# Kernel optimization log

Measured on AMD Instinct MI355X. Metric: run time of the kernel, lower is better.

The kernel has to match this reference:

```python
import jax, jax.numpy as jnp
import numpy as np

NS = [65536, 16384, 4096, 1024, 256, 64]          # nodes per level (64 = 8 graphs x 8 dense voxels)
ES = [1048576, 262144, 65536, 16384, 4096]        # edges per level (avg degree 16)
INS = [1, 15, 23, 31, 39]
OUTS = [12, 20, 28, 36, 44]
K = 5                                             # kernel_size


def setup_inputs():
    keys = iter(jax.random.split(jax.random.key(0), 64))
    d = {'x': jax.random.normal(next(keys), (NS[0], 1), jnp.float32),
         'pos': jax.random.uniform(next(keys), (NS[0], 3), jnp.float32)}
    for l in range(5):
        n, e, ci, co = NS[l], ES[l], INS[l], OUTS[l]
        d[f'src{l}'] = jax.random.randint(next(keys), (e,), 0, n)
        d[f'dst{l}'] = jax.random.randint(next(keys), (e,), 0, n)
        d[f'eattr{l}'] = jax.random.normal(next(keys), (e, 3), jnp.float32)
        d[f'cluster{l}'] = jax.random.randint(next(keys), (n,), 0, NS[l + 1])
        d[f'w1_{l}'] = jax.random.normal(next(keys), (3, K), jnp.float32) * 0.5
        d[f'b1_{l}'] = jnp.zeros((K,), jnp.float32)
        d[f'w2_{l}'] = jax.random.normal(next(keys), (K, ci * co), jnp.float32) / np.float32(np.sqrt(K * ci))
        d[f'b2_{l}'] = jnp.zeros((ci * co,), jnp.float32)
        d[f'root_{l}'] = jax.random.normal(next(keys), (ci, co), jnp.float32) / np.float32(np.sqrt(ci))
        d[f'bias_{l}'] = jnp.zeros((co,), jnp.float32)
    d['fc_w'] = jax.random.normal(next(keys), (8 * 47, 10), jnp.float32) / np.float32(np.sqrt(8 * 47))
    d['fc_b'] = jnp.zeros((10,), jnp.float32)
    return d


def _conv(x, src, dst, eattr, w1, b1, w2, b2, root, bias, n):
    # edge-conditioned kernel: MLP(edge_attr) -> [E, ci, co]
    h = jnp.tanh(eattr @ w1 + b1)                                  # [E, K]
    We = (h @ w2 + b2).reshape(eattr.shape[0], x.shape[1], -1)     # [E, ci, co]
    msg = jnp.einsum('ei,eio->eo', x[src], We)                     # gather + per-edge matvec
    s = jax.ops.segment_sum(msg, dst, num_segments=n)
    cnt = jax.ops.segment_sum(jnp.ones((dst.shape[0], 1), x.dtype), dst, num_segments=n)
    agg = s / jnp.maximum(cnt, 1.0)                                # mean aggregation
    return agg + x @ root + bias, jnp.mean(jnp.square(We))


def _pool(x, pos, cluster, n_next):
    # sparse voxel max pool on features, mean on positions; pos concatenated to features
    xm = jax.ops.segment_max(x, cluster, num_segments=n_next)
    xm = jnp.where(jnp.isfinite(xm), xm, 0.0)                      # empty voxels -> 0
    ps = jax.ops.segment_sum(pos, cluster, num_segments=n_next)
    cnt = jax.ops.segment_sum(jnp.ones((pos.shape[0], 1), pos.dtype), cluster, num_segments=n_next)
    pm = ps / jnp.maximum(cnt, 1.0)
    return jnp.concatenate([xm, pm], axis=1), pm


def reference(x, pos, src0, dst0, eattr0, cluster0, w1_0, b1_0, w2_0, b2_0, root_0, bias_0,
              src1, dst1, eattr1, cluster1, w1_1, b1_1, w2_1, b2_1, root_1, bias_1,
              src2, dst2, eattr2, cluster2, w1_2, b1_2, w2_2, b2_2, root_2, bias_2,
              src3, dst3, eattr3, cluster3, w1_3, b1_3, w2_3, b2_3, root_3, bias_3,
              src4, dst4, eattr4, cluster4, w1_4, b1_4, w2_4, b2_4, root_4, bias_4,
              fc_w, fc_b):
    lv = [(src0, dst0, eattr0, cluster0, w1_0, b1_0, w2_0, b2_0, root_0, bias_0),
          (src1, dst1, eattr1, cluster1, w1_1, b1_1, w2_1, b2_1, root_1, bias_1),
          (src2, dst2, eattr2, cluster2, w1_2, b1_2, w2_2, b2_2, root_2, bias_2),
          (src3, dst3, eattr3, cluster3, w1_3, b1_3, w2_3, b2_3, root_3, bias_3),
          (src4, dst4, eattr4, cluster4, w1_4, b1_4, w2_4, b2_4, root_4, bias_4)]
    closs = jnp.float32(0.0)
    for l, (src, dst, ea, cl, w1, b1, w2, b2, rt, bs) in enumerate(lv):
        x, c = _conv(x, src, dst, ea, w1, b1, w2, b2, rt, bs, NS[l])
        closs = closs + c
        x, pos = _pool(x, pos, cl, NS[l + 1])
    feat = x.reshape(-1, 8 * 47)                                   # [B, 8*47]
    logits = feat @ fc_w + fc_b
    return jax.nn.log_softmax(logits, axis=1), closs
```

## Files before the change

kernel.cpp:

```cpp
#include <hip/hip_runtime.h>
#include <hip/hip_fp16.h>
#include <math.h>


#define NT0   512
#define TSZ0  2048
#define NBK0  256
#define CAP0  4608
#define NT1   128
#define TSZ1  2048
#define NBK1  256
#define CAP1  1280

__device__ __forceinline__ float ftanh(float x) {
    float e = __expf(2.f * x);
    return 1.f - 2.f / (e + 1.f);
}

__device__ __forceinline__ unsigned fenc(float f) {
    int b = __float_as_int(f);
    return (b < 0) ? ~(unsigned)b : ((unsigned)b | 0x80000000u);
}
__device__ __forceinline__ float fdec(unsigned u) {
    int b = (u & 0x80000000u) ? (int)(u & 0x7fffffffu) : ~(int)u;
    return __int_as_float(b);
}

__device__ __forceinline__ float row_val(const unsigned* __restrict__ row,
                                         int i, int CI) {
    float cn = __uint_as_float(row[CI]);
    if (i < CI - 3) return (cn == 0.f) ? 0.f : fdec(row[i]);
    return __uint_as_float(row[i]) / fmaxf(cn, 1.f);
}

struct Seg4 {
    const int* idx[4];
    int*       cnt[4];
    int*       rp [4];
    int*       out[4];
    int        n  [4];
    int        nb [4];
    int        tstart[5];
};

struct GA {
    const int *src0, *dst0; const float* ea0;
    const int *src1, *dst1; const float* ea1;
    const float *x0, *pos0;
    const int* cluster[5];
    const float *w1[5], *b1[5], *w2[5], *b2[5], *root[5], *bias[5];
    const int* srcE[3]; const float* eaE[3];
    const float *fc_w, *fc_b;
    int *bcnt, *bcnt1;
    float4 *pay2, *pay1, *rec1;
    float *y0, *xn0;
    unsigned* raw[5];
    float *H, *sq;
    int *bs1, *rp1;
    Seg4 sg;
    float* out;
    int hb0[4], hsB;
};

__global__ __launch_bounds__(256) void k1_fuseA(GA A)
{
    __shared__ float4 stg[TSZ0];
    __shared__ unsigned char bkb[TSZ0];
    __shared__ int hb_[256], gb_[256], ls_[256], cu_[256];

    int B = blockIdx.x, t = threadIdx.x;

    if (B < NT0) {
        hb_[t] = 0;
        __syncthreads();
        int base = B * TSZ0 + t;
        int dreg[8];
        #pragma unroll
        for (int k = 0; k < 8; k++) {
            dreg[k] = A.dst0[base + k * 256];
            atomicAdd(&hb_[dreg[k] >> 8], 1);
        }
        __syncthreads();
        int c = hb_[t];
        gb_[t] = c ? atomicAdd(&A.bcnt[t], c) : 0;
        ls_[t] = c;
        __syncthreads();
        for (int d = 1; d < 256; d <<= 1) {
            int u = (t >= d) ? ls_[t - d] : 0;
            __syncthreads();
            ls_[t] += u;
            __syncthreads();
        }
        int ex = ls_[t] - c;
        ls_[t] = ex;
        cu_[t] = ex;
        __syncthreads();

        float w1r[15], b1r[5];
        #pragma unroll
        for (int i = 0; i < 15; i++) w1r[i] = A.w1[0][i];
        #pragma unroll
        for (int i = 0; i < 5; i++)  b1r[i] = A.b1[0][i];
        float acc[20];
        #pragma unroll
        for (int i = 0; i < 20; i++) acc[i] = 0.f;
        #pragma unroll
        for (int k = 0; k < 8; k++) {
            int i = base + k * 256;
            int d = dreg[k];
            int sv = A.src0[i];
            float e0 = A.ea0[i * 3], e1 = A.ea0[i * 3 + 1], e2 = A.ea0[i * 3 + 2];
            float h[5];
            #pragma unroll
            for (int q = 0; q < 5; q++)
                h[q] = ftanh(e0 * w1r[q] + e1 * w1r[5 + q] + e2 * w1r[10 + q] + b1r[q]);
            int p = 5;
            #pragma unroll
            for (int q = 0; q < 5; q++) {
                acc[q] += h[q];
                #pragma unroll
                for (int q2 = q; q2 < 5; q2++) acc[p++] += h[q] * h[q2];
            }
            float xv = A.x0[sv];
            union HU { __half2 h2; float f; } p01, p23;
            p01.h2 = __floats2half2_rn(h[0], h[1]);
            p23.h2 = __floats2half2_rn(h[2], h[3]);
            unsigned wbits = ((unsigned)d << 16) |
                             (unsigned)__half_as_ushort(__float2half_rn(h[4]));
            int bk = d >> 8;
            int ps = atomicAdd(&cu_[bk], 1);
            stg[ps] = make_float4(xv, p01.f, p23.f, __uint_as_float(wbits));
            bkb[ps] = (unsigned char)bk;
        }
        __syncthreads();
        #pragma unroll
        for (int k = 0; k < 8; k++) {
            int p = k * 256 + t;
            int bk = bkb[p];
            int off = gb_[bk] + (p - ls_[bk]);
            if (off < CAP0)
                A.pay2[(size_t)bk * CAP0 + off] = stg[p];
        }
        __syncthreads();
        float* red = (float*)cu_;
        int wid = t >> 6, lane = t & 63;
        #pragma unroll
        for (int v = 0; v < 20; v++) {
            float s = acc[v];
            #pragma unroll
            for (int o = 32; o; o >>= 1) s += __shfl_down(s, o);
            if (lane == 0) red[wid * 20 + v] = s;
        }
        __syncthreads();
        if (t < 20)
            atomicAdd(&A.H[t], red[t] + red[20 + t] + red[40 + t] + red[60 + t]);
        return;
    }
    B -= NT0;
    if (B < NT1) {
        hb_[t] = 0;
        __syncthreads();
        int base = B * TSZ1 + t;
        int dreg[8];
        #pragma unroll
        for (int k = 0; k < 8; k++) {
            dreg[k] = A.dst1[base + k * 256];
            atomicAdd(&hb_[dreg[k] >> 6], 1);
        }
        __syncthreads();
        int c = hb_[t];
        gb_[t] = c ? atomicAdd(&A.bcnt1[t], c) : 0;
        ls_[t] = c;
        __syncthreads();
        for (int d = 1; d < 256; d <<= 1) {
            int u = (t >= d) ? ls_[t - d] : 0;
            __syncthreads();
            ls_[t] += u;
            __syncthreads();
        }
        int ex = ls_[t] - c;
        ls_[t] = ex;
        cu_[t] = ex;
        __syncthreads();

        float w1r[15], b1r[5];
        #pragma unroll
        for (int i = 0; i < 15; i++) w1r[i] = A.w1[1][i];
        #pragma unroll
        for (int i = 0; i < 5; i++)  b1r[i] = A.b1[1][i];
        float acc[20];
        #pragma unroll
        for (int i = 0; i < 20; i++) acc[i] = 0.f;
        #pragma unroll
        for (int k = 0; k < 8; k++) {
            int i = base + k * 256;
            int d = dreg[k];
            int sv = A.src1[i];
            float e0 = A.ea1[i * 3], e1 = A.ea1[i * 3 + 1], e2 = A.ea1[i * 3 + 2];
            float h[5];
            #pragma unroll
            for (int q = 0; q < 5; q++)
                h[q] = ftanh(e0 * w1r[q] + e1 * w1r[5 + q] + e2 * w1r[10 + q] + b1r[q]);
            int p = 5;
            #pragma unroll
            for (int q = 0; q < 5; q++) {
                acc[q] += h[q];
                #pragma unroll
                for (int q2 = q; q2 < 5; q2++) acc[p++] += h[q] * h[q2];
            }
            int bk = d >> 6;
            int ps = atomicAdd(&cu_[bk], 1);
            stg[ps] = make_float4(__int_as_float((d << 16) | sv), e0, e1, e2);
            bkb[ps] = (unsigned char)bk;
        }
        __syncthreads();
        #pragma unroll
        for (int k = 0; k < 8; k++) {
            int p = k * 256 + t;
            int bk = bkb[p];
            int off = gb_[bk] + (p - ls_[bk]);
            if (off < CAP1)
                A.pay1[(size_t)bk * CAP1 + off] = stg[p];
        }
        __syncthreads();
        float* red = (float*)cu_;
        int wid = t >> 6, lane = t & 63;
        #pragma unroll
        for (int v = 0; v < 20; v++) {
            float s = acc[v];
            #pragma unroll
            for (int o = 32; o; o >>= 1) s += __shfl_down(s, o);
            if (lane == 0) red[wid * 20 + v] = s;
        }
        __syncthreads();
        if (t < 20)
            atomicAdd(&A.H[20 + t], red[t] + red[20 + t] + red[40 + t] + red[60 + t]);
        return;
    }
    B -= NT1;
    if (B < A.hsB) {
        const int K = 8;
        int j = 0;
        while (j < 2 && B >= A.hb0[j + 1]) j++;
        int bloc = B - A.hb0[j];
        const float* ea = A.eaE[j];
        const float* w1p = A.w1[j + 2];
        const float* b1p = A.b1[j + 2];
        static const int EJ[3] = {65536, 16384, 4096};
        int Ej = EJ[j];
        float w1r[15], b1r[5];
        #pragma unroll
        for (int i = 0; i < 15; i++) w1r[i] = w1p[i];
        #pragma unroll
        for (int i = 0; i < 5; i++)  b1r[i] = b1p[i];
        float acc[20];
        #pragma unroll
        for (int i = 0; i < 20; i++) acc[i] = 0.f;
        int base = bloc * 256 * K + t;
        for (int it = 0; it < K; it++) {
            int e = base + it * 256;
            if (e < Ej) {
                float e0 = ea[e * 3], e1 = ea[e * 3 + 1], e2 = ea[e * 3 + 2];
                float h[5];
                #pragma unroll
                for (int q = 0; q < 5; q++)
                    h[q] = ftanh(e0 * w1r[q] + e1 * w1r[5 + q] + e2 * w1r[10 + q] + b1r[q]);
                int p = 5;
                #pragma unroll
                for (int q = 0; q < 5; q++) {
                    acc[q] += h[q];
                    #pragma unroll
                    for (int q2 = q; q2 < 5; q2++) acc[p++] += h[q] * h[q2];
                }
            }
        }
        float* red = (float*)hb_;
        int wid = t >> 6, lane = t & 63;
        #pragma unroll
        for (int v = 0; v < 20; v++) {
            float s = acc[v];
            #pragma unroll
            for (int o = 32; o; o >>= 1) s += __shfl_down(s, o);
            if (lane == 0) red[wid * 20 + v] = s;
        }
        __syncthreads();
        if (t < 20)
            atomicAdd(&A.H[(j + 2) * 20 + t],
                      red[t] + red[20 + t] + red[40 + t] + red[60 + t]);
        return;
    }
    B -= A.hsB;
    {
        int s = 0;
        while (s < 3 && B >= A.sg.tstart[s + 1]) s++;
        int i0 = (B - A.sg.tstart[s]) * 1024;
        const int* idx = A.sg.idx[s];
        int* cnt = A.sg.cnt[s];
        int n = A.sg.n[s];
        #pragma unroll
        for (int j = 0; j < 4; j++) {
            int i = i0 + j * 256 + t;
            if (i < n) atomicAdd(&cnt[idx[i]], 1);
        }
    }
}

__global__ __launch_bounds__(256) void k2_fuseB(GA A)
{
    __shared__ float wsm[96];
    __shared__ float nacc[7 * NBK0];
    __shared__ int sc[256];
    int B = blockIdx.x, t = threadIdx.x;

    if (B < NBK0) {
        if (t < 60) wsm[t] = A.w2[0][t];
        else if (t >= 64  && t < 76)  wsm[60 + t - 64]  = A.b2[0][t - 64];
        else if (t >= 128 && t < 140) wsm[72 + t - 128] = A.root[0][t - 128];
        else if (t >= 192 && t < 204) wsm[84 + t - 192] = A.bias[0][t - 192];
        for (int u = t; u < 7 * NBK0; u += 256) nacc[u] = 0.f;
        __syncthreads();

        int n = A.bcnt[B];
        if (n > CAP0) n = CAP0;
        size_t base = (size_t)B * CAP0;
        for (int j = t; j < n; j += 256) {
            float4 R = A.pay2[base + j];
            union HU { float f; __half2 h2; } a01, a23;
            a01.f = R.y; a23.f = R.z;
            unsigned wbits = __float_as_uint(R.w);
            int rel = (int)(wbits >> 16) & 255;
            float xv = R.x;
            atomicAdd(&nacc[rel], xv);
            atomicAdd(&nacc[256 + rel],  __low2float(a01.h2)  * xv);
            atomicAdd(&nacc[512 + rel],  __high2float(a01.h2) * xv);
            atomicAdd(&nacc[768 + rel],  __low2float(a23.h2)  * xv);
            atomicAdd(&nacc[1024 + rel], __high2float(a23.h2) * xv);
            atomicAdd(&nacc[1280 + rel],
                      __half2float(__ushort_as_half((unsigned short)(wbits & 0xffffu))) * xv);
            atomicAdd(&nacc[1536 + rel], 1.f);
        }
        __syncthreads();

        int v0 = B << 8;
        for (int u = t; u < NBK0 * 12; u += 256) {
            int rel = u / 12, o = u - rel * 12;
            float dg = nacc[1536 + rel];
            float inv = 1.f / fmaxf(dg, 1.f);
            float msg = wsm[60 + o] * nacc[rel] + wsm[o] * nacc[256 + rel] +
                        wsm[12 + o] * nacc[512 + rel] + wsm[24 + o] * nacc[768 + rel] +
                        wsm[36 + o] * nacc[1024 + rel] + wsm[48 + o] * nacc[1280 + rel];
            float xv = A.x0[v0 + rel];
            A.y0[(size_t)(v0 + rel) * 12 + o] =
                msg * inv + xv * wsm[72 + o] + wsm[84 + o];
        }
        return;
    }
    B -= NBK0;
    if (B < 1) {
        int c = A.bcnt1[t];
        if (c > CAP1) c = CAP1;
        sc[t] = c;
        __syncthreads();
        for (int d = 1; d < 256; d <<= 1) {
            int u = (t >= d) ? sc[t - d] : 0;
            __syncthreads();
            sc[t] += u;
            __syncthreads();
        }
        A.bs1[t] = sc[t] - c;
        if (t == 255) { A.bs1[256] = sc[255]; A.rp1[16384] = sc[255]; }
        return;
    }
    B -= 1;
    if (B < 4) {
        int s = B;
        int nb = A.sg.nb[s];
        const int* cnt = A.sg.cnt[s];
        int* rp = A.sg.rp[s];
        int VPT = nb >> 8;
        int i0 = t * VPT;
        int sum = 0;
        for (int k = 0; k < VPT; k++) sum += cnt[i0 + k];
        int acc = sum;
        sc[t] = acc;
        __syncthreads();
        for (int d = 1; d < 256; d <<= 1) {
            int t2 = (t >= d) ? sc[t - d] : 0;
            __syncthreads();
            acc += t2;
            sc[t] = acc;
            __syncthreads();
        }
        int running = acc - sum;
        for (int k = 0; k < VPT; k++) {
            rp[i0 + k] = running;
            running += cnt[i0 + k];
        }
        if (t == 255) rp[nb] = running;
        return;
    }
    B -= 4;
    {
        if (t >= 64) return;
        int l = B;
        const float* w2l = A.w2[l];
        const float* b2l = A.b2[l];
        static const int cicoA[5] = {12, 300, 644, 1116, 1716};
        int cico = cicoA[l];
        float d[21];
        #pragma unroll
        for (int i = 0; i < 21; i++) d[i] = 0.f;
        for (int u = t; u < cico; u += 64) {
            float b = b2l[u];
            float w[5];
            #pragma unroll
            for (int k = 0; k < 5; k++) w[k] = w2l[k * cico + u];
            int p = 0;
            #pragma unroll
            for (int k = 0; k < 5; k++) {
                #pragma unroll
                for (int k2 = k; k2 < 5; k2++) d[p++] += w[k] * w[k2];
            }
            #pragma unroll
            for (int k = 0; k < 5; k++) d[15 + k] += b * w[k];
            d[20] += b * b;
        }
        #pragma unroll
        for (int i = 0; i < 21; i++) {
            #pragma unroll
            for (int off = 32; off; off >>= 1) d[i] += __shfl_down(d[i], off);
        }
        if (t == 0) {
            static const int EA[5] = {1048576, 262144, 65536, 16384, 4096};
            const float* H1 = A.H + l * 20;
            const float* H2 = H1 + 5;
            float sq = (float)EA[l] * d[20];
            #pragma unroll
            for (int k = 0; k < 5; k++) sq += 2.f * d[15 + k] * H1[k];
            int p = 0;
            #pragma unroll
            for (int k = 0; k < 5; k++) {
                #pragma unroll
                for (int k2 = k; k2 < 5; k2++) {
                    sq += ((k == k2) ? 1.f : 2.f) * d[p] * H2[p];
                    p++;
                }
            }
            A.sq[l] = sq;
        }
    }
}

__global__ __launch_bounds__(256) void k3_fuseC(GA A)
{
    __shared__ float4 st4[CAP1];
    __shared__ short  inv[CAP1];
    __shared__ int h64[64], l64[64], c64[64];
    int B = blockIdx.x, t = threadIdx.x;

    if (B < A.sg.tstart[4]) {
        int s = 0;
        while (s < 3 && B >= A.sg.tstart[s + 1]) s++;
        int i0 = (B - A.sg.tstart[s]) * 1024;
        const int* idx = A.sg.idx[s];
        int* cnt = A.sg.cnt[s];
        const int* rp = A.sg.rp[s];
        int* out = A.sg.out[s];
        int n = A.sg.n[s];
        #pragma unroll
        for (int j = 0; j < 4; j++) {
            int i = i0 + j * 256 + t;
            if (i < n) {
                int d = idx[i];
                int p = atomicSub(&cnt[d], 1) - 1;
                out[rp[d] + p] = i;
            }
        }
        return;
    }
    B -= A.sg.tstart[4];
    {
        int b = B;
        int n = A.bcnt1[b];
        if (n > CAP1) n = CAP1;
        size_t base = (size_t)b * CAP1;
        for (int j = t; j < n; j += 256) st4[j] = A.pay1[base + j];
        if (t < 64) h64[t] = 0;
        __syncthreads();
        for (int j = t; j < n; j += 256) {
            int rel = (int)(__float_as_uint(st4[j].x) >> 16) & 63;
            atomicAdd(&h64[rel], 1);
        }
        __syncthreads();
        if (t < 64) {
            int v = h64[t];
            int val = v;
            #pragma unroll
            for (int d = 1; d < 64; d <<= 1) {
                int u = __shfl_up(val, d);
                if (t >= d) val += u;
            }
            l64[t] = val - v;
            c64[t] = val - v;
        }
        __syncthreads();
        for (int j = t; j < n; j += 256) {
            int rel = (int)(__float_as_uint(st4[j].x) >> 16) & 63;
            int p = atomicAdd(&c64[rel], 1);
            inv[p] = (short)j;
        }
        __syncthreads();
        int lo = A.bs1[b];
        for (int j = t; j < n; j += 256)
            A.rec1[lo + j] = st4[inv[j]];
        if (t < 64) A.rp1[(b << 6) + t] = lo + l64[t];
    }
}

__global__ __launch_bounds__(256) void k4_pool0(GA A)
{
    int gt = blockIdx.x * 256 + threadIdx.x;
    if (gt >= 16384 * 15) return;
    int c = gt / 15, o = gt - c * 15;
    int r0 = A.sg.rp[3][c], r1 = A.sg.rp[3][c + 1];
    const int* cnid = A.sg.out[3];
    int d = r1 - r0;
    if (o < 12) {
        float m = -INFINITY;
        for (int j = r0; j < r1; j++)
            m = fmaxf(m, A.y0[(size_t)cnid[j] * 12 + o]);
        if (d == 0 || !isfinite(m)) m = 0.f;
        A.xn0[c * 15 + o] = m;
    } else {
        int k = o - 12;
        float sum = 0.f;
        for (int j = r0; j < r1; j++)
            sum += A.pos0[cnid[j] * 3 + k];
        A.xn0[c * 15 + o] = sum / fmaxf((float)d, 1.f);
    }
}

__global__ __launch_bounds__(256) void k5_conv1(GA A)
{
    constexpr int CI = 15, CO = 20, CH = 48, CICO = CI * CO, RN = 24;
    __shared__ float w1s[20];
    __shared__ float4 recb[CH];
    __shared__ int   svb[CH];
    __shared__ float hb[CH * 6];
    __shared__ float xs[CH * CI];
    __shared__ float Sx[6 * CI];
    __shared__ float xown[CI];

    int t = threadIdx.x, v = blockIdx.x;
    if (t < 20) w1s[t] = (t < 15) ? A.w1[1][t] : A.b1[1][t - 15];
    if (t < CI) xown[t] = A.xn0[v * CI + t];
    int r0 = A.rp1[v], r1 = A.rp1[v + 1];
    int d = r1 - r0;
    float acc = 0.f;

    for (int c0 = r0; c0 < r1; c0 += CH) {
        int cn = min(CH, r1 - c0);
        if (t < cn) {
            float4 R = A.rec1[c0 + t];
            recb[t] = R;
            svb[t]  = (int)(__float_as_uint(R.x) & 0xffffu);
            hb[t * 6] = 1.f;
        }
        __syncthreads();
        if (t < cn * 5) {
            int j = t / 5, k = t % 5;
            float e0 = recb[j].y, e1 = recb[j].z, e2 = recb[j].w;
            hb[j * 6 + 1 + k] =
                ftanh(e0 * w1s[k] + e1 * w1s[5 + k] + e2 * w1s[10 + k] + w1s[15 + k]);
        }
        for (int u = t; u < cn * CI; u += 256) {
            int j = u / CI, i = u - j * CI;
            xs[u] = A.xn0[svb[j] * CI + i];
        }
        __syncthreads();
        if (t < 6 * CI) {
            int i = t / 6, k6 = t - (t / 6) * 6;
            for (int j = 0; j < cn; j++)
                acc += hb[j * 6 + k6] * xs[j * CI + i];
        }
        __syncthreads();
    }

    if (t < 6 * CI) Sx[t] = acc;
    __syncthreads();

    if (t < CO) {
        float m = 0.f;
        const float* w2 = A.w2[1];
        const float* b2 = A.b2[1];
        for (int i = 0; i < CI; i++) {
            m += b2[i * CO + t] * Sx[i * 6];
            #pragma unroll
            for (int k = 0; k < 5; k++)
                m += w2[k * CICO + i * CO + t] * Sx[i * 6 + 1 + k];
        }
        m /= fmaxf((float)d, 1.f);
        for (int i = 0; i < CI; i++) m += xown[i] * A.root[1][i * CO + t];
        m += A.bias[1][t];
        int c = A.cluster[1][v];
        unsigned* orow = A.raw[1] + (size_t)c * RN;
        atomicMax(&orow[t], fenc(m));
        if (t < 3) atomicAdd((float*)&orow[CO + t], xown[CI - 3 + t]);
        if (t == 0) atomicAdd((float*)&orow[CO + 3], 1.f);
    }
}

template<int CI, int CO>
__global__ __launch_bounds__(256) void coopP_k(GA A, int l)
{
    constexpr int CH = 48, CICO = CI * CO, RL = CI + 1, RN = CO + 4;
    __shared__ float w1s[20];
    __shared__ int   eb[CH], svb[CH];
    __shared__ float hb[CH * 6];
    __shared__ float xs[CH * CI];
    __shared__ float Sx[6 * CI];
    __shared__ float xown[CI];

    int t = threadIdx.x, v = blockIdx.x;
    int s = l - 2;
    const unsigned* rin = A.raw[l - 1];
    const int* rp = A.sg.rp[s];
    const int* eid = A.sg.out[s];
    const int* src = A.srcE[s];
    const float* eattr = A.eaE[s];

    if (t < 20) w1s[t] = (t < 15) ? A.w1[l][t] : A.b1[l][t - 15];
    if (t < CI) xown[t] = row_val(rin + (size_t)v * RL, t, CI);
    int r0 = rp[v], r1 = rp[v + 1];
    int d = r1 - r0;
    float acc = 0.f;

    for (int c0 = r0; c0 < r1; c0 += CH) {
        int cn = min(CH, r1 - c0);
        if (t < cn) {
            int e = eid[c0 + t];
            eb[t]  = e;
            svb[t] = src[e];
            hb[t * 6] = 1.f;
        }
        __syncthreads();
        if (t < cn * 5) {
            int j = t / 5, k = t % 5;
            int e = eb[j];
            float e0 = eattr[e * 3], e1 = eattr[e * 3 + 1], e2 = eattr[e * 3 + 2];
            hb[j * 6 + 1 + k] =
                ftanh(e0 * w1s[k] + e1 * w1s[5 + k] + e2 * w1s[10 + k] + w1s[15 + k]);
        }
        for (int u = t; u < cn * CI; u += 256) {
            int j = u / CI, i = u - j * CI;
            xs[u] = row_val(rin + (size_t)svb[j] * RL, i, CI);
        }
        __syncthreads();
        if (t < 6 * CI) {
            int i = t / 6, k6 = t - (t / 6) * 6;
            for (int j = 0; j < cn; j++)
                acc += hb[j * 6 + k6] * xs[j * CI + i];
        }
        __syncthreads();
    }

    if (t < 6 * CI) Sx[t] = acc;
    __syncthreads();

    if (t < CO) {
        float m = 0.f;
        const float* w2 = A.w2[l];
        const float* b2 = A.b2[l];
        for (int i = 0; i < CI; i++) {
            m += b2[i * CO + t] * Sx[i * 6];
            #pragma unroll
            for (int k = 0; k < 5; k++)
                m += w2[k * CICO + i * CO + t] * Sx[i * 6 + 1 + k];
        }
        m /= fmaxf((float)d, 1.f);
        for (int i = 0; i < CI; i++) m += xown[i] * A.root[l][i * CO + t];
        m += A.bias[l][t];
        int c = A.cluster[l][v];
        unsigned* orow = A.raw[l] + (size_t)c * RN;
        atomicMax(&orow[t], fenc(m));
        if (t < 3) atomicAdd((float*)&orow[CO + t], xown[CI - 3 + t]);
        if (t == 0) atomicAdd((float*)&orow[CO + 3], 1.f);
    }
}

__global__ __launch_bounds__(128) void k9_fc(GA A)
{
    __shared__ float feat[8 * 376];
    __shared__ float logit[80];
    __shared__ float roff[8];
    const unsigned* r5 = A.raw[4];
    for (int idx = threadIdx.x; idx < 64 * 47; idx += 128) {
        int n = idx / 47, i = idx - n * 47;
        int b = n >> 3, s = n & 7;
        feat[b * 376 + s * 47 + i] = row_val(r5 + (size_t)n * 48, i, 47);
    }
    __syncthreads();
    int t = threadIdx.x;
    if (t < 80) {
        int b = t / 10, j = t % 10;
        float acc = A.fc_b[j];
        for (int k = 0; k < 376; k++) acc += feat[b * 376 + k] * A.fc_w[k * 10 + j];
        logit[t] = acc;
    }
    __syncthreads();
    if (t < 8) {
        float m = -1e30f;
        for (int j = 0; j < 10; j++) m = fmaxf(m, logit[t * 10 + j]);
        float ssum = 0.f;
        for (int j = 0; j < 10; j++) ssum += expf(logit[t * 10 + j] - m);
        roff[t] = m + logf(ssum);
    }
    __syncthreads();
    if (t < 80) A.out[t] = logit[t] - roff[t / 10];
    if (t == 0) {
        const float* sq = A.sq;
        float closs = 0.f;
        closs += sq[0] * (1.0f / 12582912.0f);
        closs += sq[1] * (1.0f / 78643200.0f);
        closs += sq[2] * (1.0f / 42205184.0f);
        closs += sq[3] * (1.0f / 18284544.0f);
        closs += sq[4] * (1.0f / 7028736.0f);
        A.out[80] = closs;
    }
}


extern "C" void kernel_launch(void* const* d_in, const int* in_sizes, int n_in,
                              void* d_out, int out_size, void* d_ws, size_t ws_size,
                              hipStream_t stream)
{
    static const int NSa[6] = {65536, 16384, 4096, 1024, 256, 64};
    static const int ESa[5] = {1048576, 262144, 65536, 16384, 4096};
    static const int RNa[5] = {16, 24, 32, 40, 48};

    int* wsw = (int*)d_ws;
    size_t off = 0;
    auto alw = [&](size_t n) -> size_t {
        size_t p = off; off += (n + 63) & ~(size_t)63; return p;
    };
    size_t degO[5];
    for (int l = 2; l < 5; l++) degO[l] = alw(NSa[l]);
    size_t cdeg0O = alw(NSa[1]);
    size_t HO    = alw(100);
    size_t bcO   = alw(NBK0);
    size_t bc1O  = alw(NBK1);
    size_t rawO[5];
    for (int l = 1; l < 5; l++) rawO[l] = alw((size_t)NSa[l + 1] * RNa[l]);
    size_t zeroWords = off;
    size_t rpO[5], eidO[5];
    for (int l = 2; l < 5; l++) rpO[l]  = alw(NSa[l] + 1);
    size_t crp0O = alw(NSa[1] + 1);
    for (int l = 2; l < 5; l++) eidO[l] = alw(ESa[l]);
    size_t cnid0O = alw(NSa[0]);
    size_t pay2O = alw((size_t)NBK0 * CAP0 * 4);
    size_t y0O   = alw((size_t)NSa[0] * 12);
    size_t xn0O  = alw((size_t)NSa[1] * 15);
    size_t bs1O  = alw(NBK1 + 1);
    size_t pay1O = alw((size_t)NBK1 * CAP1 * 4);
    size_t rec1O = alw((size_t)ESa[1] * 4);
    size_t rp1O  = alw(NSa[1] + 1);
    size_t sqO   = alw(8);

    GA A{};
    A.src0 = (const int*)d_in[2];  A.dst0 = (const int*)d_in[3];
    A.ea0  = (const float*)d_in[4];
    A.src1 = (const int*)d_in[12]; A.dst1 = (const int*)d_in[13];
    A.ea1  = (const float*)d_in[14];
    A.x0   = (const float*)d_in[0];
    A.pos0 = (const float*)d_in[1];
    for (int l = 0; l < 5; l++) {
        A.cluster[l] = (const int*)d_in[5 + 10 * l];
        A.w1[l]   = (const float*)d_in[6 + 10 * l];
        A.b1[l]   = (const float*)d_in[7 + 10 * l];
        A.w2[l]   = (const float*)d_in[8 + 10 * l];
        A.b2[l]   = (const float*)d_in[9 + 10 * l];
        A.root[l] = (const float*)d_in[10 + 10 * l];
        A.bias[l] = (const float*)d_in[11 + 10 * l];
    }
    for (int s = 0; s < 3; s++) {
        A.srcE[s] = (const int*)d_in[2 + 10 * (s + 2)];
        A.eaE[s]  = (const float*)d_in[4 + 10 * (s + 2)];
    }
    A.fc_w = (const float*)d_in[52];
    A.fc_b = (const float*)d_in[53];
    A.bcnt  = wsw + bcO;
    A.bcnt1 = wsw + bc1O;
    A.pay2 = (float4*)(wsw + pay2O);
    A.pay1 = (float4*)(wsw + pay1O);
    A.rec1 = (float4*)(wsw + rec1O);
    A.y0   = (float*)(wsw + y0O);
    A.xn0  = (float*)(wsw + xn0O);
    for (int l = 1; l < 5; l++) A.raw[l] = (unsigned*)(wsw + rawO[l]);
    A.H  = (float*)(wsw + HO);
    A.sq = (float*)(wsw + sqO);
    A.bs1 = wsw + bs1O;
    A.rp1 = wsw + rp1O;
    A.out = (float*)d_out;

    int tiles = 0;
    for (int s = 0; s < 3; s++) {
        int l = s + 2;
        A.sg.idx[s] = (const int*)d_in[3 + 10 * l];
        A.sg.cnt[s] = wsw + degO[l];
        A.sg.rp [s] = wsw + rpO[l];
        A.sg.out[s] = wsw + eidO[l];
        A.sg.n  [s] = ESa[l];
        A.sg.nb [s] = NSa[l];
        A.sg.tstart[s] = tiles;
        tiles += (ESa[l] + 1023) / 1024;
    }
    A.sg.idx[3] = (const int*)d_in[5];
    A.sg.cnt[3] = wsw + cdeg0O;
    A.sg.rp [3] = wsw + crp0O;
    A.sg.out[3] = wsw + cnid0O;
    A.sg.n  [3] = NSa[0];
    A.sg.nb [3] = NSa[1];
    A.sg.tstart[3] = tiles;
    tiles += (NSa[0] + 1023) / 1024;
    A.sg.tstart[4] = tiles;

    int hsB = 0;
    A.hb0[0] = 0;
    for (int j = 0; j < 3; j++) {
        hsB += (ESa[j + 2] + 2047) / 2048;
        A.hb0[j + 1] = hsB;
    }
    A.hsB = hsB;

    hipMemsetAsync(d_ws, 0, zeroWords * 4, stream);

    k1_fuseA<<<NT0 + NT1 + hsB + tiles, 256, 0, stream>>>(A);
    k2_fuseB<<<NBK0 + 1 + 4 + 5,        256, 0, stream>>>(A);
    k3_fuseC<<<tiles + NBK1,            256, 0, stream>>>(A);
    k4_pool0<<<(16384 * 15 + 255) / 256, 256, 0, stream>>>(A);
    k5_conv1<<<NSa[1],                  256, 0, stream>>>(A);
    coopP_k<23, 28><<<NSa[2],           256, 0, stream>>>(A, 2);
    coopP_k<31, 36><<<NSa[3],           256, 0, stream>>>(A, 3);
    coopP_k<39, 44><<<NSa[4],           256, 0, stream>>>(A, 4);
    k9_fc<<<1, 128, 0, stream>>>(A);
}
```

Baseline: 378.2 us.

## Replace shared-memory float atomics with local counting sort in level-0 aggregation

The level-0 bucket aggregation stops doing seven shared-memory float atomicAdds per edge. Instead, each 1024-edge chunk is staged in LDS, counting-sorted by destination slot, and each thread accumulates its own node's sums in registers. This removes atomic contention on hot nodes at the cost of extra barriers, a scan per chunk, and uneven per-thread loop lengths. Separately, the fourth segment's row-pointer scan (16384 counts) gets a dedicated block that stages counts in LDS for coalesced access, replacing the strided per-thread loop.

```diff
diff --git a/kernel.cpp b/kernel.cpp
--- a/kernel.cpp
+++ b/kernel.cpp
@@ -307,55 +307,105 @@
 
 __global__ __launch_bounds__(256) void k2_fuseB(GA A)
 {
-    __shared__ float wsm[96];
-    __shared__ float nacc[7 * NBK0];
-    __shared__ int sc[256];
+    __shared__ alignas(16) char poolc[34048];
     int B = blockIdx.x, t = threadIdx.x;
 
     if (B < NBK0) {
+        float4* stg = (float4*)poolc;
+        float*  Sx  = (float*)(poolc + 16384);
+        unsigned char* key = (unsigned char*)(poolc + 23552);
+        short* inv = (short*)(poolc + 24576);
+        int* hist = (int*)(poolc + 26624);
+        int* st   = (int*)(poolc + 27648);
+        int* cur  = (int*)(poolc + 28672);
+        float* wsm = (float*)(poolc + 29696);
+
         if (t < 60) wsm[t] = A.w2[0][t];
         else if (t >= 64  && t < 76)  wsm[60 + t - 64]  = A.b2[0][t - 64];
         else if (t >= 128 && t < 140) wsm[72 + t - 128] = A.root[0][t - 128];
         else if (t >= 192 && t < 204) wsm[84 + t - 192] = A.bias[0][t - 192];
-        for (int u = t; u < 7 * NBK0; u += 256) nacc[u] = 0.f;
-        __syncthreads();
 
         int n = A.bcnt[B];
         if (n > CAP0) n = CAP0;
         size_t base = (size_t)B * CAP0;
-        for (int j = t; j < n; j += 256) {
-            float4 R = A.pay2[base + j];
-            union HU { float f; __half2 h2; } a01, a23;
-            a01.f = R.y; a23.f = R.z;
-            unsigned wbits = __float_as_uint(R.w);
-            int rel = (int)(wbits >> 16) & 255;
-            float xv = R.x;
-            atomicAdd(&nacc[rel], xv);
-            atomicAdd(&nacc[256 + rel],  __low2float(a01.h2)  * xv);
-            atomicAdd(&nacc[512 + rel],  __high2float(a01.h2) * xv);
-            atomicAdd(&nacc[768 + rel],  __low2float(a23.h2)  * xv);
-            atomicAdd(&nacc[1024 + rel], __high2float(a23.h2) * xv);
-            atomicAdd(&nacc[1280 + rel],
-                      __half2float(__ushort_as_half((unsigned short)(wbits & 0xffffu))) * xv);
-            atomicAdd(&nacc[1536 + rel], 1.f);
-        }
-        __syncthreads();
-
+        float s0 = 0.f, s1 = 0.f, s2 = 0.f, s3 = 0.f, s4 = 0.f, s5 = 0.f, dg = 0.f;
+
+        for (int c0 = 0; c0 < n; c0 += 1024) {
+            int cn = min(1024, n - c0);
+            hist[t] = 0;
+            __syncthreads();
+            #pragma unroll
+            for (int k = 0; k < 4; k++) {
+                int j = k * 256 + t;
+                if (j < cn) {
+                    float4 R = A.pay2[base + c0 + j];
+                    stg[j] = R;
+                    int rel = (int)(__float_as_uint(R.w) >> 16) & 255;
+                    key[j] = (unsigned char)rel;
+                    atomicAdd(&hist[rel], 1);
+                }
+            }
+            __syncthreads();
+            int h = hist[t];
+            int acc = h;
+            st[t] = acc;
+            __syncthreads();
+            for (int d = 1; d < 256; d <<= 1) {
+                int u = (t >= d) ? st[t - d] : 0;
+                __syncthreads();
+                acc += u;
+                st[t] = acc;
+                __syncthreads();
+            }
+            int ex = acc - h;
+            st[t] = ex;
+            cur[t] = ex;
+            __syncthreads();
+            #pragma unroll
+            for (int k = 0; k < 4; k++) {
+                int j = k * 256 + t;
+                if (j < cn) {
+                    int p = atomicAdd(&cur[key[j]], 1);
+                    inv[p] = (short)j;
+                }
+            }
+            __syncthreads();
+            for (int q = st[t]; q < cur[t]; q++) {
+                float4 R = stg[inv[q]];
+                union HU { float f; __half2 h2; } a01, a23;
+                a01.f = R.y; a23.f = R.z;
+                unsigned wbits = __float_as_uint(R.w);
+                float xv = R.x;
+                s0 += xv;
+                s1 += __low2float(a01.h2)  * xv;
+                s2 += __high2float(a01.h2) * xv;
+                s3 += __low2float(a23.h2)  * xv;
+                s4 += __high2float(a23.h2) * xv;
+                s5 += __half2float(__ushort_as_half((unsigned short)(wbits & 0xffffu))) * xv;
+                dg += 1.f;
+            }
+            __syncthreads();
+        }
+        Sx[t] = s0;        Sx[256 + t] = s1;  Sx[512 + t] = s2;
+        Sx[768 + t] = s3;  Sx[1024 + t] = s4; Sx[1280 + t] = s5;
+        Sx[1536 + t] = dg;
+        __syncthreads();
         int v0 = B << 8;
-        for (int u = t; u < NBK0 * 12; u += 256) {
+        for (int u = t; u < 256 * 12; u += 256) {
             int rel = u / 12, o = u - rel * 12;
-            float dg = nacc[1536 + rel];
-            float inv = 1.f / fmaxf(dg, 1.f);
-            float msg = wsm[60 + o] * nacc[rel] + wsm[o] * nacc[256 + rel] +
-                        wsm[12 + o] * nacc[512 + rel] + wsm[24 + o] * nacc[768 + rel] +
-                        wsm[36 + o] * nacc[1024 + rel] + wsm[48 + o] * nacc[1280 + rel];
+            float dgv = Sx[1536 + rel];
+            float invd = 1.f / fmaxf(dgv, 1.f);
+            float msg = wsm[60 + o] * Sx[rel] + wsm[o] * Sx[256 + rel] +
+                        wsm[12 + o] * Sx[512 + rel] + wsm[24 + o] * Sx[768 + rel] +
+                        wsm[36 + o] * Sx[1024 + rel] + wsm[48 + o] * Sx[1280 + rel];
             float xv = A.x0[v0 + rel];
             A.y0[(size_t)(v0 + rel) * 12 + o] =
-                msg * inv + xv * wsm[72 + o] + wsm[84 + o];
+                msg * invd + xv * wsm[72 + o] + wsm[84 + o];
         }
         return;
     }
     B -= NBK0;
+    int* sc = (int*)poolc;
     if (B < 1) {
         int c = A.bcnt1[t];
         if (c > CAP1) c = CAP1;
@@ -372,7 +422,7 @@
         return;
     }
     B -= 1;
-    if (B < 4) {
+    if (B < 3) {
         int s = B;
         int nb = A.sg.nb[s];
         const int* cnt = A.sg.cnt[s];
@@ -399,7 +449,52 @@
         if (t == 255) rp[nb] = running;
         return;
     }
-    B -= 4;
+    B -= 3;
+    if (B < 1) {
+        int* big = (int*)poolc;
+        int* scx = (int*)(poolc + 32768);
+        int* tot = (int*)(poolc + 33792);
+        const int* cnt = A.sg.cnt[3];
+        int* rp = A.sg.rp[3];
+        int carry = 0;
+        for (int p = 0; p < 2; p++) {
+            if (p == 1) carry = tot[0];
+            #pragma unroll
+            for (int k = 0; k < 32; k++)
+                big[k * 256 + t] = cnt[p * 8192 + k * 256 + t];
+            __syncthreads();
+            int b0 = t * 32;
+            int s = 0;
+            #pragma unroll
+            for (int j = 0; j < 32; j++) s += big[b0 + j];
+            int acc = s;
+            scx[t] = acc;
+            __syncthreads();
+            for (int d = 1; d < 256; d <<= 1) {
+                int u = (t >= d) ? scx[t - d] : 0;
+                __syncthreads();
+                acc += u;
+                scx[t] = acc;
+                __syncthreads();
+            }
+            if (t == 255) tot[0] = carry + acc;
+            int run = carry + acc - s;
+            #pragma unroll
+            for (int j = 0; j < 32; j++) {
+                int v = big[b0 + j];
+                big[b0 + j] = run;
+                run += v;
+            }
+            __syncthreads();
+            #pragma unroll
+            for (int k = 0; k < 32; k++)
+                rp[p * 8192 + k * 256 + t] = big[k * 256 + t];
+            __syncthreads();
+        }
+        if (t == 255) rp[16384] = tot[0];
+        return;
+    }
+    B -= 1;
     {
         if (t >= 64) return;
         int l = B;
@@ -835,7 +930,7 @@
     hipMemsetAsync(d_ws, 0, zeroWords * 4, stream);
 
     k1_fuseA<<<NT0 + NT1 + hsB + tiles, 256, 0, stream>>>(A);
-    k2_fuseB<<<NBK0 + 1 + 4 + 5,        256, 0, stream>>>(A);
+    k2_fuseB<<<NBK0 + 1 + 3 + 1 + 5,    256, 0, stream>>>(A);
     k3_fuseC<<<tiles + NBK1,            256, 0, stream>>>(A);
     k4_pool0<<<(16384 * 15 + 255) / 256, 256, 0, stream>>>(A);
     k5_conv1<<<NSa[1],                  256, 0, stream>>>(A);
```

Result: faster. 342.1 us, median of 2 (-9.5%).
